# Kernel optimization log

Measured on AMD Instinct MI355X. Metric: run time of the kernel, lower is better.

## Reference

```python
import jax, jax.numpy as jnp
import numpy as np

EMBED_DIM = 256; N_HEADS = 8; HEAD_DIM = 32; N_PAIRS = 16
POS_DIM = 2; N_LEVELS = 4; NBH = [3, 5, 7, 9]
N_Q = 2048; BATCH = 2; FULL = 128
SPATIAL_THETA = 100.0; LEVEL_THETA = 10.0
LN_EPS = 1e-5


def _grids():
    offs, lvls = [], []
    for l, s in enumerate(NBH):
        ax = np.arange(s)
        g = np.stack(np.meshgrid(ax, ax, indexing='ij'), -1).reshape(-1, 2)
        offs.append(g - (s - 1) // 2)
        lvls.append(np.full(s * s, l))
    return (np.concatenate(offs).astype(np.int32), np.concatenate(lvls).astype(np.int32))

OFFSETS, LEVEL_IDS = _grids()  # [164,2], [164]
K_PER_Q = OFFSETS.shape[0]


def _apply_rope(x, pos, freqs):
    # x: [..., n_heads, n_pairs, 2]; pos: [..., 3]; freqs: [3, n_pairs]
    ang = pos @ freqs                      # [..., n_pairs]
    c = jnp.cos(ang)[..., None, :]         # broadcast over heads
    s = jnp.sin(ang)[..., None, :]
    x1, x2 = x[..., 0], x[..., 1]
    return jnp.stack([x1 * c - x2 * s, x1 * s + x2 * c], axis=-1)


def setup_inputs() -> dict:
    key = jax.random.key(0)
    ks = jax.random.split(key, 8)
    scale = EMBED_DIM ** -0.5
    i = jnp.arange(N_PAIRS, dtype=jnp.float32) / N_PAIRS
    rope_freqs = jnp.stack([SPATIAL_THETA ** -i, SPATIAL_THETA ** -i, LEVEL_THETA ** -i])  # [3,16]
    level_spatial_shapes = jnp.array([[FULL >> l, FULL >> l] for l in range(N_LEVELS)], jnp.int32)
    return {
        'query': jax.random.normal(ks[0], (N_Q, EMBED_DIM), jnp.float32),
        'query_spatial_positions': jax.random.uniform(ks[1], (N_Q, POS_DIM), jnp.float32) * (FULL - 1),
        'stacked_feature_maps': jax.random.normal(ks[2], (BATCH, N_LEVELS, FULL, FULL, EMBED_DIM), jnp.float32) * 0.02,
        'norm_w': jnp.ones((EMBED_DIM,), jnp.float32),
        'norm_b': jnp.zeros((EMBED_DIM,), jnp.float32),
        'q_w': jax.random.normal(ks[3], (EMBED_DIM, EMBED_DIM), jnp.float32) * scale,
        'k_w': jax.random.normal(ks[4], (EMBED_DIM, EMBED_DIM), jnp.float32) * scale,
        'v_w': jax.random.normal(ks[5], (EMBED_DIM, EMBED_DIM), jnp.float32) * scale,
        'out_w': jax.random.normal(ks[6], (EMBED_DIM, EMBED_DIM), jnp.float32) * scale,
        'rope_freqs': rope_freqs,
        'query_batch_offsets': jnp.array([0, N_Q // 2, N_Q], jnp.int32),
        'level_spatial_shapes': level_spatial_shapes,
    }


def reference(query, query_spatial_positions, stacked_feature_maps, norm_w, norm_b,
              q_w, k_w, v_w, out_w, rope_freqs, query_batch_offsets, level_spatial_shapes):
    n_q = query.shape[0]
    residual = query

    # pre-LayerNorm
    mu = query.mean(-1, keepdims=True)
    var = query.var(-1, keepdims=True)
    x = (query - mu) * jax.lax.rsqrt(var + LN_EPS) * norm_w + norm_b

    # query projection + RoPE (spatial dims + level dim; queries sit at max-res level 0)
    q = x @ q_w
    qpos = jnp.concatenate([query_spatial_positions, jnp.zeros((n_q, 1), query.dtype)], -1)  # [n_q,3]
    q_rot = _apply_rope(q.reshape(n_q, N_HEADS, N_PAIRS, 2), qpos, rope_freqs).reshape(n_q, N_HEADS, HEAD_DIM)

    # multilevel neighborhood indices
    shapes_f = level_spatial_shapes.astype(query.dtype)               # [L,2]
    scaling = shapes_f / shapes_f.max(0)                              # [L,2]
    scaled = query_spatial_positions[:, None, :] * scaling[None]      # [n_q,L,2]
    centers = jnp.floor(scaled).astype(jnp.int32)                     # [n_q,L,2]
    lvl = jnp.asarray(LEVEL_IDS)                                      # [K]
    idx = centers[:, lvl, :] + jnp.asarray(OFFSETS)[None]             # [n_q,K,2]
    lsh = level_spatial_shapes[lvl]                                   # [K,2]
    valid = jnp.all((idx >= 0) & (idx < lsh[None]), -1)               # [n_q,K]
    idxc = jnp.clip(idx, 0, lsh[None] - 1)

    # per-query batch ids from offsets
    b = jnp.searchsorted(query_batch_offsets, jnp.arange(n_q, dtype=query_batch_offsets.dtype), side='right') - 1

    # sparse gather of key/value features (unspecified -> zero)
    feats = stacked_feature_maps[b[:, None], lvl[None, :], idxc[..., 0], idxc[..., 1]]  # [n_q,K,E]
    feats = feats * valid[..., None].astype(feats.dtype)

    k = feats @ k_w
    v = feats @ v_w

    # key positions at full scale + level coordinate
    stride = (shapes_f.max(0)[None] / shapes_f)[lvl]                  # [K,2]
    kpos_sp = (idx.astype(query.dtype) + 0.5) * stride[None]          # [n_q,K,2]
    kpos = jnp.concatenate([kpos_sp, jnp.broadcast_to(lvl.astype(query.dtype), (n_q, K_PER_Q))[..., None]], -1)
    k_rot = _apply_rope(k.reshape(n_q, K_PER_Q, N_HEADS, N_PAIRS, 2), kpos, rope_freqs)
    k_rot = k_rot.reshape(n_q, K_PER_Q, N_HEADS, HEAD_DIM)

    # attention over the 164 gathered keys per query
    logits = jnp.einsum('nhd,nkhd->nhk', q_rot, k_rot) / np.sqrt(HEAD_DIM)
    logits = jnp.where(valid[:, None, :], logits, jnp.asarray(-1e9, logits.dtype))
    attn = jax.nn.softmax(logits, axis=-1)
    out = jnp.einsum('nhk,nkhd->nhd', attn, v.reshape(n_q, K_PER_Q, N_HEADS, HEAD_DIM))
    out = out.reshape(n_q, EMBED_DIM) @ out_w
    return out + residual
```

## Files before the change

### kernel.cpp

```cpp
#include <hip/hip_runtime.h>
#include <hip/hip_bf16.h>

typedef unsigned short u16;
typedef short short8 __attribute__((ext_vector_type(8)));
typedef float f32x4 __attribute__((ext_vector_type(4)));

#define ROWS_PER_BATCH 21760
#define TOT_ROWS 43520

__device__ __forceinline__ u16 f2bf(float f){
  unsigned u = __builtin_bit_cast(unsigned, f);
  u += 0x7FFFu + ((u >> 16) & 1u);
  return (u16)(u >> 16);
}
__device__ __forceinline__ float bf2f(u16 h){
  return __builtin_bit_cast(float, ((unsigned)h) << 16);
}
__device__ __forceinline__ float bflo(unsigned u){ return __builtin_bit_cast(float, u << 16); }
__device__ __forceinline__ float bfhi(unsigned u){ return __builtin_bit_cast(float, u & 0xFFFF0000u); }
__device__ __forceinline__ unsigned pk2bf(float a, float b){
  __hip_bfloat162 h = __float22bfloat162_rn(make_float2(a, b));
  union { __hip_bfloat162 h2; unsigned u; } cv; cv.h2 = h; return cv.u;
}

__global__ __launch_bounds__(256) void wt_kernel(
    const float* __restrict__ qw, const float* __restrict__ kw,
    const float* __restrict__ vw, const float* __restrict__ ow,
    u16* __restrict__ wtq, u16* __restrict__ wtk,
    u16* __restrict__ wtv, u16* __restrict__ wto){
  int t = blockIdx.x * 256 + threadIdx.x;
  int which = t >> 13;
  int r = t & 8191;
  int cg = r >> 9;
  int kk = (r >> 6) & 7;
  int lane = r & 63;
  int quad = lane >> 4, mn = lane & 15;
  const float* s = which == 0 ? qw : which == 1 ? kw : which == 2 ? vw : ow;
  u16* d       = which == 0 ? wtq : which == 1 ? wtk : which == 2 ? wtv : wto;
  const float* base = s + (kk * 32 + quad * 8) * 256 + cg * 16 + mn;
  float e[8];
  #pragma unroll
  for (int j = 0; j < 8; ++j) e[j] = base[j * 256];
  uint4 o = { pk2bf(e[0], e[1]), pk2bf(e[2], e[3]), pk2bf(e[4], e[5]), pk2bf(e[6], e[7]) };
  *(uint4*)(d + (size_t)r * 8) = o;
}

__global__ __launch_bounds__(256) void ln_kernel(
    const float* __restrict__ q, const float* __restrict__ w,
    const float* __restrict__ b, u16* __restrict__ x){
  const int t = threadIdx.x;
  const int row = blockIdx.x * 4 + (t >> 6);
  const int lane = t & 63;
  const float4 v = *(const float4*)(q + (size_t)row * 256 + lane * 4);
  float s1 = v.x + v.y + v.z + v.w;
  float s2 = v.x*v.x + v.y*v.y + v.z*v.z + v.w*v.w;
  #pragma unroll
  for (int o = 32; o > 0; o >>= 1){
    s1 += __shfl_xor(s1, o);
    s2 += __shfl_xor(s2, o);
  }
  float mu = s1 * (1.0f / 256.0f);
  float var = s2 * (1.0f / 256.0f) - mu * mu;
  float rs = rsqrtf(var + 1e-5f);
  const float4 wv = *(const float4*)(w + lane * 4);
  const float4 bv = *(const float4*)(b + lane * 4);
  float o0 = (v.x - mu) * rs * wv.x + bv.x;
  float o1 = (v.y - mu) * rs * wv.y + bv.y;
  float o2 = (v.z - mu) * rs * wv.z + bv.z;
  float o3 = (v.w - mu) * rs * wv.w + bv.w;
  uint2 pk = { pk2bf(o0, o1), pk2bf(o2, o3) };
  *(uint2*)(x + (size_t)row * 256 + lane * 4) = pk;
}

__global__ __launch_bounds__(256) void kv_gemm(const float* __restrict__ fm,
        const u16* __restrict__ wtkp, const u16* __restrict__ wtvp,
        const float* __restrict__ rope,
        u16* __restrict__ krot, u16* __restrict__ vmap){
  __shared__ __align__(16) char smraw[33792];
  u16 (*Alds)[264] = (u16 (*)[264])smraw;
  typedef float eslab[16][66];
  eslab* epil = (eslab*)smraw;
  __shared__ unsigned sh_cs[64][16];

  const int t = threadIdx.x;
  const int row0 = blockIdx.x * 64;

  const int b = row0 / ROWS_PER_BATCH;
  const int rr = row0 - b * ROWS_PER_BATCH;
  int l, loff;
  if (rr < 16384)      { l = 0; loff = 0; }
  else if (rr < 20480) { l = 1; loff = 16384; }
  else if (rr < 21504) { l = 2; loff = 20480; }
  else                 { l = 3; loff = 21504; }
  const int logW = 7 - l;
  const int Wm1 = (128 >> l) - 1;
  const int cell0 = rr - loff;
  const float* fmbase = fm + (size_t)(b * 4 + l) * (128 * 128 * 256);

  for (int i = 0; i < 16; ++i){
    int chunk = i * 256 + t;
    int lr = chunk >> 6;
    int c4 = chunk & 63;
    int cell = cell0 + lr;
    int y = cell >> logW;
    int x = cell & Wm1;
    const float4 v = *(const float4*)(fmbase + ((((y << 7) + x) << 8) + c4 * 4));
    uint2 pk = { pk2bf(v.x, v.y), pk2bf(v.z, v.w) };
    *(uint2*)&Alds[lr][c4 * 4] = pk;
  }
  #pragma unroll
  for (int i = 0; i < 4; ++i){
    int id = i * 256 + t;
    int lr = id >> 4, p = id & 15;
    int cell = cell0 + lr;
    int i0 = cell >> logW;
    int i1 = cell & Wm1;
    float fs = (float)(1 << l);
    float kx = ((float)i0 + 0.5f) * fs;
    float ky = ((float)i1 + 0.5f) * fs;
    float ang = kx * rope[p] + ky * rope[16 + p] + (float)l * rope[32 + p];
    sh_cs[lr][p] = pk2bf(__cosf(ang), __sinf(ang));
  }
  __syncthreads();

  const int wv = t >> 6;
  const int lane = t & 63;
  const int mn = lane & 15;
  const int quad = lane >> 4;

  short8 af[8];
  #pragma unroll
  for (int kk = 0; kk < 8; ++kk)
    af[kk] = *(const short8*)&Alds[wv * 16 + mn][kk * 32 + quad * 8];
  __syncthreads();

  for (int m = 0; m < 2; ++m){
    const u16* wt = m ? wtvp : wtkp;
    u16* outp = m ? vmap : krot;
    for (int cs2 = 0; cs2 < 4; ++cs2){
      f32x4 acc[4];
      #pragma unroll
      for (int i = 0; i < 4; ++i) acc[i] = (f32x4){0.f, 0.f, 0.f, 0.f};
      for (int kk = 0; kk < 8; ++kk){
        #pragma unroll
        for (int tile = 0; tile < 4; ++tile){
          const short8 bfr = *(const short8*)(wt +
              ((size_t)(((cs2 * 4 + tile) * 8 + kk) * 64 + lane)) * 8);
          acc[tile] = __builtin_amdgcn_mfma_f32_16x16x32_bf16(af[kk], bfr, acc[tile], 0, 0, 0);
        }
      }
      const int par = (m * 4 + cs2) & 1;
      float (*sl)[66] = epil[par * 4 + wv];
      #pragma unroll
      for (int tile = 0; tile < 4; ++tile)
        #pragma unroll
        for (int r = 0; r < 4; ++r)
          sl[quad * 4 + r][tile * 16 + mn] = acc[tile][r];
      __syncthreads();
      #pragma unroll
      for (int i = 0; i < 8; ++i){
        int pi = i * 64 + lane;
        int row = pi >> 5;
        int pl = pi & 31;
        float2 kv2 = *(const float2*)&sl[row][pl * 2];
        unsigned o;
        if (m == 0){
          unsigned csn = sh_cs[wv * 16 + row][pl & 15];
          float c = bflo(csn), s = bfhi(csn);
          o = pk2bf(kv2.x * c - kv2.y * s, kv2.x * s + kv2.y * c);
        } else {
          o = pk2bf(kv2.x, kv2.y);
        }
        *(unsigned*)(outp + (size_t)(row0 + wv * 16 + row) * 256 + cs2 * 64 + pl * 2) = o;
      }
    }
  }
}

__global__ __launch_bounds__(256) void gemm_xw(const u16* __restrict__ A,
        const u16* __restrict__ wt, const float* __restrict__ resid,
        float* __restrict__ out){
  __shared__ u16 Alds[64][264];
  const int t = threadIdx.x;
  const int row0 = blockIdx.x * 64;
  #pragma unroll
  for (int i = 0; i < 8; ++i){
    int chunk = i * 256 + t;
    int lr = chunk >> 5;
    int c8 = chunk & 31;
    uint4 v = *(const uint4*)(A + (size_t)(row0 + lr) * 256 + c8 * 8);
    *(uint4*)&Alds[lr][c8 * 8] = v;
  }
  __syncthreads();
  const int wv = t >> 6;
  const int lane = t & 63;
  const int mn = lane & 15;
  const int quad = lane >> 4;
  f32x4 acc[2];
  acc[0] = (f32x4){0.f,0.f,0.f,0.f};
  acc[1] = (f32x4){0.f,0.f,0.f,0.f};
  for (int kk = 0; kk < 8; ++kk){
    short8 a = *(const short8*)&Alds[wv * 16 + mn][kk * 32 + quad * 8];
    #pragma unroll
    for (int tile = 0; tile < 2; ++tile){
      int cg = blockIdx.y * 2 + tile;
      const short8 bfr = *(const short8*)(wt + ((size_t)((cg * 8 + kk) * 64 + lane)) * 8);
      acc[tile] = __builtin_amdgcn_mfma_f32_16x16x32_bf16(a, bfr, acc[tile], 0, 0, 0);
    }
  }
  #pragma unroll
  for (int tile = 0; tile < 2; ++tile){
    int col = blockIdx.y * 32 + tile * 16 + mn;
    #pragma unroll
    for (int r = 0; r < 4; ++r){
      int row = row0 + wv * 16 + quad * 4 + r;
      float val = acc[tile][r];
      if (resid) val += resid[(size_t)row * 256 + col];
      out[(size_t)row * 256 + col] = val;
    }
  }
}

__global__ __launch_bounds__(256) void attn2(
    const float* __restrict__ qraw, const float* __restrict__ qsp,
    const float* __restrict__ rope, const int* __restrict__ qbo, int nbo,
    const u16* __restrict__ krot, const u16* __restrict__ vmap,
    u16* __restrict__ ao){
  __shared__ float sh_q[8][33];
  __shared__ float sh_lg[8][168];
  __shared__ int   sh_row[176];
  const int t = threadIdx.x;
  const int qi = blockIdx.x;

  int bidx = 0;
  for (int j = 1; j < nbo; ++j) if (qi >= qbo[j]) bidx = j;
  const float p0 = qsp[qi * 2 + 0];
  const float p1 = qsp[qi * 2 + 1];

  {
    float qv = qraw[(size_t)qi * 256 + t];
    int p = (t & 31) >> 1;
    float ang = p0 * rope[p] + p1 * rope[16 + p];
    float c = __cosf(ang), s = __sinf(ang);
    float partner = __shfl_xor(qv, 1);
    float val = (t & 1) ? (partner * s + qv * c) : (qv * c - partner * s);
    sh_q[t >> 5][t & 31] = val * 0.17677669529663687f;
  }

  if (t < 164){
    int l, dy, dx, loff;
    if (t < 9)       { l = 0; int j = t;      dy = j / 3 - 1; dx = j % 3 - 1; loff = 0; }
    else if (t < 34) { l = 1; int j = t - 9;  dy = j / 5 - 2; dx = j % 5 - 2; loff = 16384; }
    else if (t < 83) { l = 2; int j = t - 34; dy = j / 7 - 3; dx = j % 7 - 3; loff = 20480; }
    else             { l = 3; int j = t - 83; dy = j / 9 - 4; dx = j % 9 - 4; loff = 21504; }
    float sc = 1.0f / (float)(1 << l);
    int i0 = (int)floorf(p0 * sc) + dy;
    int i1 = (int)floorf(p1 * sc) + dx;
    int W = 128 >> l;
    sh_row[t] = (i0 < 0 || i0 >= W || i1 < 0 || i1 >= W)
              ? -1 : bidx * ROWS_PER_BATCH + loff + (i0 << (7 - l)) + i1;
  }
  __syncthreads();

  const int h = t & 7;
  const int kbase = t >> 3;
  float qreg[32];
  #pragma unroll
  for (int d = 0; d < 32; ++d) qreg[d] = sh_q[h][d];
  for (int pass = 0; pass < 6; ++pass){
    int kk = pass * 32 + kbase;
    if (kk < 164){
      int row = sh_row[kk];
      float lg = -1e9f;
      if (row >= 0){
        const uint4* kp = (const uint4*)(krot + (size_t)row * 256 + h * 32);
        uint4 A0 = kp[0], A1 = kp[1], A2 = kp[2], A3 = kp[3];
        unsigned uu[16];
        uu[0]=A0.x; uu[1]=A0.y; uu[2]=A0.z; uu[3]=A0.w;
        uu[4]=A1.x; uu[5]=A1.y; uu[6]=A1.z; uu[7]=A1.w;
        uu[8]=A2.x; uu[9]=A2.y; uu[10]=A2.z; uu[11]=A2.w;
        uu[12]=A3.x; uu[13]=A3.y; uu[14]=A3.z; uu[15]=A3.w;
        lg = 0.f;
        #pragma unroll
        for (int j = 0; j < 16; ++j)
          lg += qreg[2*j] * bflo(uu[j]) + qreg[2*j+1] * bfhi(uu[j]);
      }
      sh_lg[h][kk] = lg;
    }
  }
  __syncthreads();

  const int h3 = t >> 5;
  const int l32 = t & 31;
  float m = -1e30f;
  for (int kk = l32; kk < 164; kk += 32) m = fmaxf(m, sh_lg[h3][kk]);
  #pragma unroll
  for (int o = 16; o > 0; o >>= 1) m = fmaxf(m, __shfl_xor(m, o));
  float ssum = 0.f;
  for (int kk = l32; kk < 164; kk += 32){
    float e = __expf(sh_lg[h3][kk] - m);
    sh_lg[h3][kk] = e;
    ssum += e;
  }
  #pragma unroll
  for (int o = 16; o > 0; o >>= 1) ssum += __shfl_xor(ssum, o);
  const float inv = 1.0f / ssum;
  __syncthreads();

  float acc = 0.f;
  #pragma unroll 4
  for (int kk = 0; kk < 164; ++kk){
    int row = sh_row[kk];
    int rc = row < 0 ? 0 : row;
    float e = sh_lg[h3][kk];
    acc += e * bf2f(vmap[(size_t)rc * 256 + t]);
  }
  ao[(size_t)qi * 256 + t] = f2bf(acc * inv);
}

extern "C" void kernel_launch(void* const* d_in, const int* in_sizes, int n_in,
                              void* d_out, int out_size, void* d_ws, size_t ws_size,
                              hipStream_t stream) {
  (void)n_in; (void)out_size; (void)ws_size;
  const float* query  = (const float*)d_in[0];
  const float* qsp    = (const float*)d_in[1];
  const float* fm     = (const float*)d_in[2];
  const float* norm_w = (const float*)d_in[3];
  const float* norm_b = (const float*)d_in[4];
  const float* q_w    = (const float*)d_in[5];
  const float* k_w    = (const float*)d_in[6];
  const float* v_w    = (const float*)d_in[7];
  const float* out_w  = (const float*)d_in[8];
  const float* rope   = (const float*)d_in[9];
  const int*   qbo    = (const int*)d_in[10];
  float* out = (float*)d_out;
  const int n_q = in_sizes[0] / 256;
  const int nbo = in_sizes[10];

  char* p = (char*)d_ws;
  u16* krot = (u16*)p;                       p += (size_t)TOT_ROWS * 256 * 2;
  u16* vmap = (u16*)p;                       p += (size_t)TOT_ROWS * 256 * 2;
  float* qraw = (float*)p;                   p += (size_t)n_q * 256 * 4;
  u16* xbf = (u16*)p;                        p += (size_t)n_q * 256 * 2;
  u16* wtq = (u16*)p;                        p += 65536 * 2;
  u16* wtk = (u16*)p;                        p += 65536 * 2;
  u16* wtv = (u16*)p;                        p += 65536 * 2;
  u16* wto = (u16*)p;
  u16* ao = xbf;

  hipLaunchKernelGGL(wt_kernel, dim3(128), dim3(256), 0, stream,
                     q_w, k_w, v_w, out_w, wtq, wtk, wtv, wto);
  hipLaunchKernelGGL(ln_kernel, dim3(n_q / 4), dim3(256), 0, stream,
                     query, norm_w, norm_b, xbf);
  hipLaunchKernelGGL(kv_gemm, dim3(TOT_ROWS / 64), dim3(256), 0, stream,
                     fm, wtk, wtv, rope, krot, vmap);
  hipLaunchKernelGGL(gemm_xw, dim3(n_q / 64, 8), dim3(256), 0, stream,
                     xbf, wtq, (const float*)nullptr, qraw);
  hipLaunchKernelGGL(attn2, dim3(n_q), dim3(256), 0, stream,
                     qraw, qsp, rope, qbo, nbo, krot, vmap, ao);
  hipLaunchKernelGGL(gemm_xw, dim3(n_q / 64, 8), dim3(256), 0, stream,
                     ao, wto, query, out);
}
```

Baseline: 308.1 us.

## Merge prep kernels, split KV GEMM across grid, prefetch weights, vectorize PV

```diff
diff --git a/kernel.cpp b/kernel.cpp
--- a/kernel.cpp
+++ b/kernel.cpp
@@ -23,67 +23,69 @@
   union { __hip_bfloat162 h2; unsigned u; } cv; cv.h2 = h; return cv.u;
 }
 
-__global__ __launch_bounds__(256) void wt_kernel(
+__global__ __launch_bounds__(256) void prep_kernel(
     const float* __restrict__ qw, const float* __restrict__ kw,
     const float* __restrict__ vw, const float* __restrict__ ow,
+    const float* __restrict__ q, const float* __restrict__ nw,
+    const float* __restrict__ nb,
     u16* __restrict__ wtq, u16* __restrict__ wtk,
-    u16* __restrict__ wtv, u16* __restrict__ wto){
-  int t = blockIdx.x * 256 + threadIdx.x;
-  int which = t >> 13;
-  int r = t & 8191;
-  int cg = r >> 9;
-  int kk = (r >> 6) & 7;
-  int lane = r & 63;
-  int quad = lane >> 4, mn = lane & 15;
-  const float* s = which == 0 ? qw : which == 1 ? kw : which == 2 ? vw : ow;
-  u16* d       = which == 0 ? wtq : which == 1 ? wtk : which == 2 ? wtv : wto;
-  const float* base = s + (kk * 32 + quad * 8) * 256 + cg * 16 + mn;
-  float e[8];
-  #pragma unroll
-  for (int j = 0; j < 8; ++j) e[j] = base[j * 256];
-  uint4 o = { pk2bf(e[0], e[1]), pk2bf(e[2], e[3]), pk2bf(e[4], e[5]), pk2bf(e[6], e[7]) };
-  *(uint4*)(d + (size_t)r * 8) = o;
-}
-
-__global__ __launch_bounds__(256) void ln_kernel(
-    const float* __restrict__ q, const float* __restrict__ w,
-    const float* __restrict__ b, u16* __restrict__ x){
+    u16* __restrict__ wtv, u16* __restrict__ wto, u16* __restrict__ x){
+  const int bx = blockIdx.x;
   const int t = threadIdx.x;
-  const int row = blockIdx.x * 4 + (t >> 6);
-  const int lane = t & 63;
-  const float4 v = *(const float4*)(q + (size_t)row * 256 + lane * 4);
-  float s1 = v.x + v.y + v.z + v.w;
-  float s2 = v.x*v.x + v.y*v.y + v.z*v.z + v.w*v.w;
-  #pragma unroll
-  for (int o = 32; o > 0; o >>= 1){
-    s1 += __shfl_xor(s1, o);
-    s2 += __shfl_xor(s2, o);
-  }
-  float mu = s1 * (1.0f / 256.0f);
-  float var = s2 * (1.0f / 256.0f) - mu * mu;
-  float rs = rsqrtf(var + 1e-5f);
-  const float4 wv = *(const float4*)(w + lane * 4);
-  const float4 bv = *(const float4*)(b + lane * 4);
-  float o0 = (v.x - mu) * rs * wv.x + bv.x;
-  float o1 = (v.y - mu) * rs * wv.y + bv.y;
-  float o2 = (v.z - mu) * rs * wv.z + bv.z;
-  float o3 = (v.w - mu) * rs * wv.w + bv.w;
-  uint2 pk = { pk2bf(o0, o1), pk2bf(o2, o3) };
-  *(uint2*)(x + (size_t)row * 256 + lane * 4) = pk;
-}
-
-__global__ __launch_bounds__(256) void kv_gemm(const float* __restrict__ fm,
+  if (bx < 128){
+    int e = bx * 256 + t;
+    int which = e >> 13;
+    int r = e & 8191;
+    int cg = r >> 9;
+    int kk = (r >> 6) & 7;
+    int lane = r & 63;
+    int quad = lane >> 4, mn = lane & 15;
+    const float* s = which == 0 ? qw : which == 1 ? kw : which == 2 ? vw : ow;
+    u16* d       = which == 0 ? wtq : which == 1 ? wtk : which == 2 ? wtv : wto;
+    const float* base = s + (kk * 32 + quad * 8) * 256 + cg * 16 + mn;
+    float e8[8];
+    #pragma unroll
+    for (int j = 0; j < 8; ++j) e8[j] = base[j * 256];
+    uint4 o = { pk2bf(e8[0], e8[1]), pk2bf(e8[2], e8[3]),
+                pk2bf(e8[4], e8[5]), pk2bf(e8[6], e8[7]) };
+    *(uint4*)(d + (size_t)r * 8) = o;
+  } else {
+    const int row = (bx - 128) * 4 + (t >> 6);
+    const int lane = t & 63;
+    const float4 v = *(const float4*)(q + (size_t)row * 256 + lane * 4);
+    float s1 = v.x + v.y + v.z + v.w;
+    float s2 = v.x*v.x + v.y*v.y + v.z*v.z + v.w*v.w;
+    #pragma unroll
+    for (int o = 32; o > 0; o >>= 1){
+      s1 += __shfl_xor(s1, o);
+      s2 += __shfl_xor(s2, o);
+    }
+    float mu = s1 * (1.0f / 256.0f);
+    float var = s2 * (1.0f / 256.0f) - mu * mu;
+    float rs = rsqrtf(var + 1e-5f);
+    const float4 wv = *(const float4*)(nw + lane * 4);
+    const float4 bv = *(const float4*)(nb + lane * 4);
+    float o0 = (v.x - mu) * rs * wv.x + bv.x;
+    float o1 = (v.y - mu) * rs * wv.y + bv.y;
+    float o2 = (v.z - mu) * rs * wv.z + bv.z;
+    float o3 = (v.w - mu) * rs * wv.w + bv.w;
+    uint2 pk = { pk2bf(o0, o1), pk2bf(o2, o3) };
+    *(uint2*)(x + (size_t)row * 256 + lane * 4) = pk;
+  }
+}
+
+__global__ __launch_bounds__(256, 4) void kv_gemm(const float* __restrict__ fm,
         const u16* __restrict__ wtkp, const u16* __restrict__ wtvp,
         const float* __restrict__ rope,
         u16* __restrict__ krot, u16* __restrict__ vmap){
-  __shared__ __align__(16) char smraw[33792];
-  u16 (*Alds)[264] = (u16 (*)[264])smraw;
-  typedef float eslab[16][66];
-  eslab* epil = (eslab*)smraw;
-  __shared__ unsigned sh_cs[64][16];
+  __shared__ float slab[4][16][66];
+  __shared__ unsigned sh_cs[4][16][16];
 
   const int t = threadIdx.x;
   const int row0 = blockIdx.x * 64;
+  const int m = blockIdx.y;
+  const u16* wtp = m ? wtvp : wtkp;
+  u16* outp = m ? vmap : krot;
 
   const int b = row0 / ROWS_PER_BATCH;
   const int rr = row0 - b * ROWS_PER_BATCH;
@@ -97,82 +99,85 @@
   const int cell0 = rr - loff;
   const float* fmbase = fm + (size_t)(b * 4 + l) * (128 * 128 * 256);
 
-  for (int i = 0; i < 16; ++i){
-    int chunk = i * 256 + t;
-    int lr = chunk >> 6;
-    int c4 = chunk & 63;
-    int cell = cell0 + lr;
-    int y = cell >> logW;
-    int x = cell & Wm1;
-    const float4 v = *(const float4*)(fmbase + ((((y << 7) + x) << 8) + c4 * 4));
-    uint2 pk = { pk2bf(v.x, v.y), pk2bf(v.z, v.w) };
-    *(uint2*)&Alds[lr][c4 * 4] = pk;
-  }
-  #pragma unroll
-  for (int i = 0; i < 4; ++i){
-    int id = i * 256 + t;
-    int lr = id >> 4, p = id & 15;
-    int cell = cell0 + lr;
-    int i0 = cell >> logW;
-    int i1 = cell & Wm1;
-    float fs = (float)(1 << l);
-    float kx = ((float)i0 + 0.5f) * fs;
-    float ky = ((float)i1 + 0.5f) * fs;
-    float ang = kx * rope[p] + ky * rope[16 + p] + (float)l * rope[32 + p];
-    sh_cs[lr][p] = pk2bf(__cosf(ang), __sinf(ang));
-  }
-  __syncthreads();
-
   const int wv = t >> 6;
   const int lane = t & 63;
   const int mn = lane & 15;
   const int quad = lane >> 4;
 
   short8 af[8];
-  #pragma unroll
-  for (int kk = 0; kk < 8; ++kk)
-    af[kk] = *(const short8*)&Alds[wv * 16 + mn][kk * 32 + quad * 8];
-  __syncthreads();
-
-  for (int m = 0; m < 2; ++m){
-    const u16* wt = m ? wtvp : wtkp;
-    u16* outp = m ? vmap : krot;
-    for (int cs2 = 0; cs2 < 4; ++cs2){
-      f32x4 acc[4];
+  {
+    int cell = cell0 + wv * 16 + mn;
+    int y = cell >> logW, x = cell & Wm1;
+    const float* arow = fmbase + (((y << 7) + x) << 8) + quad * 8;
+    #pragma unroll
+    for (int kk = 0; kk < 8; ++kk){
+      float4 a0 = *(const float4*)(arow + kk * 32);
+      float4 a1 = *(const float4*)(arow + kk * 32 + 4);
+      union { short8 s; uint4 u; } cv;
+      cv.u = (uint4){ pk2bf(a0.x, a0.y), pk2bf(a0.z, a0.w),
+                      pk2bf(a1.x, a1.y), pk2bf(a1.z, a1.w) };
+      af[kk] = cv.s;
+    }
+  }
+
+  if (m == 0){
+    #pragma unroll
+    for (int i = 0; i < 4; ++i){
+      int id = i * 64 + lane;
+      int lr = id >> 4, p = id & 15;
+      int cell = cell0 + wv * 16 + lr;
+      int i0 = cell >> logW;
+      int i1 = cell & Wm1;
+      float fs = (float)(1 << l);
+      float kx = ((float)i0 + 0.5f) * fs;
+      float ky = ((float)i1 + 0.5f) * fs;
+      float ang = kx * rope[p] + ky * rope[16 + p] + (float)l * rope[32 + p];
+      sh_cs[wv][lr][p] = pk2bf(__cosf(ang), __sinf(ang));
+    }
+  }
+
+  for (int cs2 = 0; cs2 < 4; ++cs2){
+    const u16* wb = wtp + (size_t)((cs2 * 4 * 8) * 64 + lane) * 8;
+    short8 bc[4], bn[4];
+    #pragma unroll
+    for (int tl = 0; tl < 4; ++tl)
+      bc[tl] = *(const short8*)(wb + (size_t)(tl * 8) * 64 * 8);
+    f32x4 acc[4];
+    #pragma unroll
+    for (int i = 0; i < 4; ++i) acc[i] = (f32x4){0.f, 0.f, 0.f, 0.f};
+    #pragma unroll
+    for (int kk = 0; kk < 8; ++kk){
+      if (kk < 7){
+        #pragma unroll
+        for (int tl = 0; tl < 4; ++tl)
+          bn[tl] = *(const short8*)(wb + (size_t)(tl * 8 + kk + 1) * 64 * 8);
+      }
       #pragma unroll
-      for (int i = 0; i < 4; ++i) acc[i] = (f32x4){0.f, 0.f, 0.f, 0.f};
-      for (int kk = 0; kk < 8; ++kk){
-        #pragma unroll
-        for (int tile = 0; tile < 4; ++tile){
-          const short8 bfr = *(const short8*)(wt +
-              ((size_t)(((cs2 * 4 + tile) * 8 + kk) * 64 + lane)) * 8);
-          acc[tile] = __builtin_amdgcn_mfma_f32_16x16x32_bf16(af[kk], bfr, acc[tile], 0, 0, 0);
-        }
+      for (int tl = 0; tl < 4; ++tl)
+        acc[tl] = __builtin_amdgcn_mfma_f32_16x16x32_bf16(af[kk], bc[tl], acc[tl], 0, 0, 0);
+      #pragma unroll
+      for (int tl = 0; tl < 4; ++tl) bc[tl] = bn[tl];
+    }
+    #pragma unroll
+    for (int tl = 0; tl < 4; ++tl)
+      #pragma unroll
+      for (int r = 0; r < 4; ++r)
+        slab[wv][quad * 4 + r][tl * 16 + mn] = acc[tl][r];
+    #pragma unroll
+    for (int i = 0; i < 8; ++i){
+      int pi = i * 64 + lane;
+      int row = pi >> 5;
+      int pl = pi & 31;
+      float2 kv2 = *(const float2*)&slab[wv][row][pl * 2];
+      unsigned o;
+      if (m == 0){
+        unsigned csn = sh_cs[wv][row][pl & 15];
+        float c = bflo(csn), s = bfhi(csn);
+        o = pk2bf(kv2.x * c - kv2.y * s, kv2.x * s + kv2.y * c);
+      } else {
+        o = pk2bf(kv2.x, kv2.y);
       }
-      const int par = (m * 4 + cs2) & 1;
-      float (*sl)[66] = epil[par * 4 + wv];
-      #pragma unroll
-      for (int tile = 0; tile < 4; ++tile)
-        #pragma unroll
-        for (int r = 0; r < 4; ++r)
-          sl[quad * 4 + r][tile * 16 + mn] = acc[tile][r];
-      __syncthreads();
-      #pragma unroll
-      for (int i = 0; i < 8; ++i){
-        int pi = i * 64 + lane;
-        int row = pi >> 5;
-        int pl = pi & 31;
-        float2 kv2 = *(const float2*)&sl[row][pl * 2];
-        unsigned o;
-        if (m == 0){
-          unsigned csn = sh_cs[wv * 16 + row][pl & 15];
-          float c = bflo(csn), s = bfhi(csn);
-          o = pk2bf(kv2.x * c - kv2.y * s, kv2.x * s + kv2.y * c);
-        } else {
-          o = pk2bf(kv2.x, kv2.y);
-        }
-        *(unsigned*)(outp + (size_t)(row0 + wv * 16 + row) * 256 + cs2 * 64 + pl * 2) = o;
-      }
+      *(unsigned*)(outp + (size_t)(row0 + wv * 16 + row) * 256 + cs2 * 64 + pl * 2) = o;
     }
   }
 }
@@ -180,44 +185,38 @@
 __global__ __launch_bounds__(256) void gemm_xw(const u16* __restrict__ A,
         const u16* __restrict__ wt, const float* __restrict__ resid,
         float* __restrict__ out){
-  __shared__ u16 Alds[64][264];
   const int t = threadIdx.x;
-  const int row0 = blockIdx.x * 64;
-  #pragma unroll
-  for (int i = 0; i < 8; ++i){
-    int chunk = i * 256 + t;
-    int lr = chunk >> 5;
-    int c8 = chunk & 31;
-    uint4 v = *(const uint4*)(A + (size_t)(row0 + lr) * 256 + c8 * 8);
-    *(uint4*)&Alds[lr][c8 * 8] = v;
-  }
-  __syncthreads();
+  const int row0 = blockIdx.x * 16;
   const int wv = t >> 6;
   const int lane = t & 63;
   const int mn = lane & 15;
   const int quad = lane >> 4;
-  f32x4 acc[2];
-  acc[0] = (f32x4){0.f,0.f,0.f,0.f};
-  acc[1] = (f32x4){0.f,0.f,0.f,0.f};
+  const int cg = blockIdx.y * 4 + wv;
+
+  short8 af[8];
+  {
+    const u16* arow = A + (size_t)(row0 + mn) * 256 + quad * 8;
+    #pragma unroll
+    for (int kk = 0; kk < 8; ++kk)
+      af[kk] = *(const short8*)(arow + kk * 32);
+  }
+  const u16* wb = wt + (size_t)((cg * 8) * 64 + lane) * 8;
+  short8 bc = *(const short8*)wb;
+  f32x4 acc = (f32x4){0.f, 0.f, 0.f, 0.f};
+  #pragma unroll
   for (int kk = 0; kk < 8; ++kk){
-    short8 a = *(const short8*)&Alds[wv * 16 + mn][kk * 32 + quad * 8];
-    #pragma unroll
-    for (int tile = 0; tile < 2; ++tile){
-      int cg = blockIdx.y * 2 + tile;
-      const short8 bfr = *(const short8*)(wt + ((size_t)((cg * 8 + kk) * 64 + lane)) * 8);
-      acc[tile] = __builtin_amdgcn_mfma_f32_16x16x32_bf16(a, bfr, acc[tile], 0, 0, 0);
-    }
-  }
-  #pragma unroll
-  for (int tile = 0; tile < 2; ++tile){
-    int col = blockIdx.y * 32 + tile * 16 + mn;
-    #pragma unroll
-    for (int r = 0; r < 4; ++r){
-      int row = row0 + wv * 16 + quad * 4 + r;
-      float val = acc[tile][r];
-      if (resid) val += resid[(size_t)row * 256 + col];
-      out[(size_t)row * 256 + col] = val;
-    }
+    short8 bn;
+    if (kk < 7) bn = *(const short8*)(wb + (size_t)(kk + 1) * 64 * 8);
+    acc = __builtin_amdgcn_mfma_f32_16x16x32_bf16(af[kk], bc, acc, 0, 0, 0);
+    bc = bn;
+  }
+  const int col = cg * 16 + mn;
+  #pragma unroll
+  for (int r = 0; r < 4; ++r){
+    int row = row0 + quad * 4 + r;
+    float val = acc[r];
+    if (resid) val += resid[(size_t)row * 256 + col];
+    out[(size_t)row * 256 + col] = val;
   }
 }
 
@@ -229,6 +228,8 @@
   __shared__ float sh_q[8][33];
   __shared__ float sh_lg[8][168];
   __shared__ int   sh_row[176];
+  __shared__ float sh_inv[8];
+  __shared__ float sh_pv[2][128][2];
   const int t = threadIdx.x;
   const int qi = blockIdx.x;
 
@@ -292,30 +293,47 @@
 
   const int h3 = t >> 5;
   const int l32 = t & 31;
-  float m = -1e30f;
-  for (int kk = l32; kk < 164; kk += 32) m = fmaxf(m, sh_lg[h3][kk]);
-  #pragma unroll
-  for (int o = 16; o > 0; o >>= 1) m = fmaxf(m, __shfl_xor(m, o));
+  float mx = -1e30f;
+  for (int kk = l32; kk < 164; kk += 32) mx = fmaxf(mx, sh_lg[h3][kk]);
+  #pragma unroll
+  for (int o = 16; o > 0; o >>= 1) mx = fmaxf(mx, __shfl_xor(mx, o));
   float ssum = 0.f;
   for (int kk = l32; kk < 164; kk += 32){
-    float e = __expf(sh_lg[h3][kk] - m);
+    float e = __expf(sh_lg[h3][kk] - mx);
     sh_lg[h3][kk] = e;
     ssum += e;
   }
   #pragma unroll
   for (int o = 16; o > 0; o >>= 1) ssum += __shfl_xor(ssum, o);
-  const float inv = 1.0f / ssum;
+  if (l32 == 0) sh_inv[h3] = 1.0f / ssum;
   __syncthreads();
 
-  float acc = 0.f;
-  #pragma unroll 4
-  for (int kk = 0; kk < 164; ++kk){
-    int row = sh_row[kk];
-    int rc = row < 0 ? 0 : row;
-    float e = sh_lg[h3][kk];
-    acc += e * bf2f(vmap[(size_t)rc * 256 + t]);
-  }
-  ao[(size_t)qi * 256 + t] = f2bf(acc * inv);
+  {
+    const int half = t >> 7;
+    const int d2 = t & 127;
+    const int hh = d2 >> 4;
+    float a0 = 0.f, a1 = 0.f;
+    const int k0 = half * 82;
+    #pragma unroll 4
+    for (int kk = k0; kk < k0 + 82; ++kk){
+      int row = sh_row[kk];
+      int rc = row < 0 ? 0 : row;
+      unsigned vv = *(const unsigned*)(vmap + (size_t)rc * 256 + d2 * 2);
+      float e = sh_lg[hh][kk];
+      a0 += e * bflo(vv);
+      a1 += e * bfhi(vv);
+    }
+    sh_pv[half][d2][0] = a0;
+    sh_pv[half][d2][1] = a1;
+  }
+  __syncthreads();
+  if (t < 128){
+    const int hh = t >> 4;
+    float inv = sh_inv[hh];
+    float o0 = (sh_pv[0][t][0] + sh_pv[1][t][0]) * inv;
+    float o1 = (sh_pv[0][t][1] + sh_pv[1][t][1]) * inv;
+    *(unsigned*)(ao + (size_t)qi * 256 + t * 2) = pk2bf(o0, o1);
+  }
 }
 
 extern "C" void kernel_launch(void* const* d_in, const int* in_sizes, int n_in,
@@ -348,16 +366,15 @@
   u16* wto = (u16*)p;
   u16* ao = xbf;
 
-  hipLaunchKernelGGL(wt_kernel, dim3(128), dim3(256), 0, stream,
-                     q_w, k_w, v_w, out_w, wtq, wtk, wtv, wto);
-  hipLaunchKernelGGL(ln_kernel, dim3(n_q / 4), dim3(256), 0, stream,
-                     query, norm_w, norm_b, xbf);
-  hipLaunchKernelGGL(kv_gemm, dim3(TOT_ROWS / 64), dim3(256), 0, stream,
+  hipLaunchKernelGGL(prep_kernel, dim3(128 + n_q / 4), dim3(256), 0, stream,
+                     q_w, k_w, v_w, out_w, query, norm_w, norm_b,
+                     wtq, wtk, wtv, wto, xbf);
+  hipLaunchKernelGGL(kv_gemm, dim3(TOT_ROWS / 64, 2), dim3(256), 0, stream,
                      fm, wtk, wtv, rope, krot, vmap);
-  hipLaunchKernelGGL(gemm_xw, dim3(n_q / 64, 8), dim3(256), 0, stream,
+  hipLaunchKernelGGL(gemm_xw, dim3(n_q / 16, 4), dim3(256), 0, stream,
                      xbf, wtq, (const float*)nullptr, qraw);
   hipLaunchKernelGGL(attn2, dim3(n_q), dim3(256), 0, stream,
                      qraw, qsp, rope, qbo, nbo, krot, vmap, ao);
-  hipLaunchKernelGGL(gemm_xw, dim3(n_q / 64, 8), dim3(256), 0, stream,
+  hipLaunchKernelGGL(gemm_xw, dim3(n_q / 16, 4), dim3(256), 0, stream,
                      ao, wto, query, out);
 }
```

Result: faster. 281.2 us (-8.7%).
